# Optimization experiments

Hardware: AMD Instinct MI355X
Metric: run time of the kernel (lower is better)

## Reference

```python
import jax, jax.numpy as jnp
import numpy as np

BANDWIDTHS = (1e-2, 1e-1, 1e0, 1e1)  # params = [{'bandwidth': 10**i} for i in range(-2, 2)]


def setup_inputs() -> dict:
    key = jax.random.key(0)
    kx, ky = jax.random.split(key)
    n, d = 6144, 16
    X = jax.random.normal(kx, (n, d), dtype=jnp.float32)
    Y = jax.random.normal(ky, (n, d), dtype=jnp.float32)
    return {"X": X, "Y": Y}


def reference(X, Y):
    n_x, n_y = X.shape[0], Y.shape[0]
    M = jnp.concatenate([X, Y], axis=0)                     # [n_x+n_y, d]
    sq = jnp.sum(M * M, axis=1)                             # [N]
    D = sq[:, None] + sq[None, :] - 2.0 * (M @ M.T)         # squared pairwise dists [N,N]
    D = jnp.maximum(D, 0.0)
    # SumKernels over 4 RBF bandwidths: K = sum_b exp(-D / (2*bw^2))
    K = jnp.zeros_like(D)
    for bw in BANDWIDTHS:
        K = K + jnp.exp(-D / (2.0 * bw * bw))
    # cross_average biased mask S = outer(s, s) with s = [1/n_x,...,-1/n_y,...];
    # (S*K).sum() == s^T K s, computed without materializing S.
    s = jnp.concatenate([jnp.full((n_x,), 1.0 / n_x, dtype=M.dtype),
                         jnp.full((n_y,), -1.0 / n_y, dtype=M.dtype)])
    return jnp.einsum('i,ij,j->', s, K, s)
```

## Files before the change

### kernel.cpp

```cpp
#include <hip/hip_runtime.h>


using bf16x8 = __attribute__((ext_vector_type(8))) __bf16;
using f32x16 = __attribute__((ext_vector_type(16))) float;

constexpr int DIM   = 16;
constexpr int PTILE = 128;
constexpr int BLOCK = 256;
constexpr int CHUNK = 3;

constexpr float C1f = 0.72134752044448170f;
constexpr float C2f = 0.0072134752044448170f;

__device__ __forceinline__ float exp2_fast(float x) {
    float r; asm("v_exp_f32 %0, %1" : "=v"(r) : "v"(x)); return r;
}
__device__ __forceinline__ f32x16 zf() {
    f32x16 z;
#pragma unroll
    for (int i = 0; i < 16; ++i) z[i] = 0.f;
    return z;
}
__device__ __forceinline__ float sq4(float4 v) {
    return v.x*v.x + v.y*v.y + v.z*v.z + v.w*v.w;
}

__global__ __launch_bounds__(256) void mmd_prep(
    const float* __restrict__ X, const float* __restrict__ Y, int nx, int N,
    bf16x8* __restrict__ hi, bf16x8* __restrict__ lo, float* __restrict__ sq)
{
    int pt = blockIdx.x * blockDim.x + threadIdx.x;
    if (pt >= N) return;
    const float* row = (pt < nx) ? (X + (size_t)pt * DIM)
                                 : (Y + (size_t)(pt - nx) * DIM);
    const float4* r4 = reinterpret_cast<const float4*>(row);
    float4 u0 = r4[0], u1 = r4[1], u2 = r4[2], u3 = r4[3];
    float v[16] = {u0.x,u0.y,u0.z,u0.w, u1.x,u1.y,u1.z,u1.w,
                   u2.x,u2.y,u2.z,u2.w, u3.x,u3.y,u3.z,u3.w};
    float s = sq4(u0) + sq4(u1) + sq4(u2) + sq4(u3);

    bf16x8 H0, H1, L0, L1;
#pragma unroll
    for (int k = 0; k < 8; ++k) {
        __bf16 h0 = (__bf16)v[k];
        __bf16 h1 = (__bf16)v[k + 8];
        H0[k] = h0; H1[k] = h1;
        L0[k] = (__bf16)(v[k]     - (float)h0);
        L1[k] = (__bf16)(v[k + 8] - (float)h1);
    }
    int g = pt >> 5, p = pt & 31;
    hi[(g*2 + 0)*32 + p] = H0;
    hi[(g*2 + 1)*32 + p] = H1;
    lo[(g*2 + 0)*32 + p] = L0;
    lo[(g*2 + 1)*32 + p] = L1;
    sq[pt] = s;
}

struct Buf {
    bf16x8 aH0, aH1, aL0, aL1, bH0, bH1, bL0, bL1;
    float qa0[16], qa1[16];
    float qb0, qb1;
    float scale;
    int mode;
};

#define EPI_FULL(ACC, QA, QB) do { \
    _Pragma("unroll") \
    for (int q = 0; q < 16; ++q) { \
        float dd = fmaf(-2.f, ACC[q], QA[q] + QB); \
        accA += exp2_fast(-C1f * dd); \
        accB += exp2_fast(-C2f * dd); \
    } } while (0)

#define EPI_MASK(ACC, QA, QB) do { \
    _Pragma("unroll") \
    for (int q = 0; q < 16; ++q) { \
        float dd = fmaf(-2.f, ACC[q], QA[q] + QB); \
        float e1 = exp2_fast(-C1f * dd); \
        float e2 = exp2_fast(-C2f * dd); \
        bool m = l31 > (4*lh + (q & 3) + 8*(q >> 2)); \
        accA += m ? e1 : 0.f; \
        accB += m ? e2 : 0.f; \
    } } while (0)

__global__ __launch_bounds__(BLOCK, 2) void mmd_pairs3(
    const bf16x8* __restrict__ hi, const bf16x8* __restrict__ lo,
    const float*  __restrict__ sq, int nx, int T, int npairs,
    float wxf, float wynf, double* __restrict__ partials)
{
    __shared__ double wsums[BLOCK / 64];
    const int tid = threadIdx.x, w = tid >> 6, lane = tid & 63;
    const int wr = w >> 1, wc = w & 1, l31 = lane & 31, lh = lane >> 5;
    const int fo = lh * 32 + l31;

    float acc_run = 0.f;
    Buf B0, B1;

    auto issue = [&](int p, Buf& B) {
        if (p >= npairs) { B.mode = 3; return; }
        double A = (double)(2 * T + 1);
        int ti = (int)((A - sqrt(A * A - 8.0 * (double)p)) * 0.5);
        while ((ti + 1) * (2 * T + 1 - (ti + 1)) / 2 <= p) ++ti;
        while (ti * (2 * T + 1 - ti) / 2 > p) --ti;
        int tj = ti + (p - ti * (2 * T + 1 - ti) / 2);
        bool dg = (ti == tj);
        B.mode = dg ? ((wr > wc) ? 2 : ((wr == wc) ? 1 : 0)) : 0;
        int i0 = ti * PTILE, j0 = tj * PTILE;
        float wi = (i0 < nx) ? wxf : wynf;
        float wj = (j0 < nx) ? wxf : wynf;
        B.scale = wi * wj;
        if (B.mode == 2) return;
        int ga = ti * 4 + 2 * wr, gb = tj * 4 + 2 * wc;
        B.aH0 = hi[(ga + 0) * 64 + fo]; B.aH1 = hi[(ga + 1) * 64 + fo];
        B.aL0 = lo[(ga + 0) * 64 + fo]; B.aL1 = lo[(ga + 1) * 64 + fo];
        B.bH0 = hi[(gb + 0) * 64 + fo]; B.bH1 = hi[(gb + 1) * 64 + fo];
        B.bL0 = lo[(gb + 0) * 64 + fo]; B.bL1 = lo[(gb + 1) * 64 + fo];
        const float4* s4 = reinterpret_cast<const float4*>(sq);
        int rb0 = ((ga + 0) * 32 + 4 * lh) >> 2;
        int rb1 = ((ga + 1) * 32 + 4 * lh) >> 2;
        float4 t0 = s4[rb0 + 0], t1 = s4[rb0 + 2], t2 = s4[rb0 + 4], t3 = s4[rb0 + 6];
        float4 u0 = s4[rb1 + 0], u1 = s4[rb1 + 2], u2 = s4[rb1 + 4], u3 = s4[rb1 + 6];
        B.qa0[0]=t0.x;  B.qa0[1]=t0.y;  B.qa0[2]=t0.z;  B.qa0[3]=t0.w;
        B.qa0[4]=t1.x;  B.qa0[5]=t1.y;  B.qa0[6]=t1.z;  B.qa0[7]=t1.w;
        B.qa0[8]=t2.x;  B.qa0[9]=t2.y;  B.qa0[10]=t2.z; B.qa0[11]=t2.w;
        B.qa0[12]=t3.x; B.qa0[13]=t3.y; B.qa0[14]=t3.z; B.qa0[15]=t3.w;
        B.qa1[0]=u0.x;  B.qa1[1]=u0.y;  B.qa1[2]=u0.z;  B.qa1[3]=u0.w;
        B.qa1[4]=u1.x;  B.qa1[5]=u1.y;  B.qa1[6]=u1.z;  B.qa1[7]=u1.w;
        B.qa1[8]=u2.x;  B.qa1[9]=u2.y;  B.qa1[10]=u2.z; B.qa1[11]=u2.w;
        B.qa1[12]=u3.x; B.qa1[13]=u3.y; B.qa1[14]=u3.z; B.qa1[15]=u3.w;
        B.qb0 = sq[(gb + 0) * 32 + l31];
        B.qb1 = sq[(gb + 1) * 32 + l31];
    };

    auto compute = [&](Buf& B) {
        if (B.mode >= 2) return;
        f32x16 a00 = zf(), a01 = zf(), a10 = zf(), a11 = zf();
        a00 = __builtin_amdgcn_mfma_f32_32x32x16_bf16(B.aL0, B.bH0, a00, 0,0,0);
        a01 = __builtin_amdgcn_mfma_f32_32x32x16_bf16(B.aL0, B.bH1, a01, 0,0,0);
        a10 = __builtin_amdgcn_mfma_f32_32x32x16_bf16(B.aL1, B.bH0, a10, 0,0,0);
        a11 = __builtin_amdgcn_mfma_f32_32x32x16_bf16(B.aL1, B.bH1, a11, 0,0,0);
        a00 = __builtin_amdgcn_mfma_f32_32x32x16_bf16(B.aH0, B.bL0, a00, 0,0,0);
        a01 = __builtin_amdgcn_mfma_f32_32x32x16_bf16(B.aH0, B.bL1, a01, 0,0,0);
        a10 = __builtin_amdgcn_mfma_f32_32x32x16_bf16(B.aH1, B.bL0, a10, 0,0,0);
        a11 = __builtin_amdgcn_mfma_f32_32x32x16_bf16(B.aH1, B.bL1, a11, 0,0,0);
        a00 = __builtin_amdgcn_mfma_f32_32x32x16_bf16(B.aH0, B.bH0, a00, 0,0,0);
        a01 = __builtin_amdgcn_mfma_f32_32x32x16_bf16(B.aH0, B.bH1, a01, 0,0,0);
        a10 = __builtin_amdgcn_mfma_f32_32x32x16_bf16(B.aH1, B.bH0, a10, 0,0,0);
        a11 = __builtin_amdgcn_mfma_f32_32x32x16_bf16(B.aH1, B.bH1, a11, 0,0,0);

        float accA = 0.f, accB = 0.f;
        if (B.mode == 1) {
            EPI_MASK(a00, B.qa0, B.qb0);
            EPI_FULL(a01, B.qa0, B.qb1);
            EPI_MASK(a11, B.qa1, B.qb1);
        } else {
            EPI_FULL(a00, B.qa0, B.qb0);
            EPI_FULL(a01, B.qa0, B.qb1);
            EPI_FULL(a10, B.qa1, B.qb0);
            EPI_FULL(a11, B.qa1, B.qb1);
        }
        acc_run = fmaf(B.scale, accA + accB, acc_run);
    };

    const int base = blockIdx.x * CHUNK;
    issue(base + 0, B0);
    issue(base + 1, B1);
    compute(B0);
    issue(base + 2, B0);
    compute(B1);
    compute(B0);

    float tot = acc_run;
#pragma unroll
    for (int off = 32; off > 0; off >>= 1) tot += __shfl_down(tot, off);
    if (lane == 0) wsums[w] = (double)tot;
    __syncthreads();
    if (tid == 0)
        partials[blockIdx.x] = wsums[0] + wsums[1] + wsums[2] + wsums[3];
}

__global__ void mmd_reduce(const double* __restrict__ partials, int nb,
                           float* __restrict__ out, double diagv)
{
    __shared__ double sh[256];
    double s = 0.0;
    for (int i = threadIdx.x; i < nb; i += 256) s += partials[i];
    sh[threadIdx.x] = s;
    __syncthreads();
    for (int st = 128; st > 0; st >>= 1) {
        if (threadIdx.x < st) sh[threadIdx.x] += sh[threadIdx.x + st];
        __syncthreads();
    }
    if (threadIdx.x == 0) out[0] = (float)(2.0 * sh[0] + diagv);
}

__global__ void mmd_finalize(const double* __restrict__ acc,
                             float* __restrict__ out, double diag)
{
    out[0] = (float)(2.0 * acc[0] + diag);
}

constexpr int FTILE = 256;
constexpr int FBLOCK = 128;
__global__ __launch_bounds__(FBLOCK, 4) void mmd_pairs_fb(
    const float* __restrict__ Xp, const float* __restrict__ Yp,
    int nx, int T, double wx, double wyn, double* __restrict__ acc_out)
{
    __shared__ float  bs[FTILE][DIM];
    __shared__ float  bsq[FTILE];
    __shared__ double wsums[FBLOCK / 64];
    int ti = 0;
    int rem = blockIdx.x;
    while (rem >= T - ti) { rem -= (T - ti); ++ti; }
    int tj = ti + rem;
    const int i0 = ti * FTILE, j0 = tj * FTILE;
    const float* bbase = (j0 < nx) ? (Xp + (size_t)j0 * DIM) : (Yp + (size_t)(j0 - nx) * DIM);
    const float* abase = (i0 < nx) ? (Xp + (size_t)i0 * DIM) : (Yp + (size_t)(i0 - nx) * DIM);
    for (int r = threadIdx.x; r < FTILE; r += FBLOCK) {
        const float4* rp = reinterpret_cast<const float4*>(bbase + (size_t)r * DIM);
        float4 v0 = rp[0], v1 = rp[1], v2 = rp[2], v3 = rp[3];
        float4* sp = reinterpret_cast<float4*>(&bs[r][0]);
        sp[0]=v0; sp[1]=v1; sp[2]=v2; sp[3]=v3;
        bsq[r] = sq4(v0)+sq4(v1)+sq4(v2)+sq4(v3);
    }
    float a0[DIM], a1[DIM], sqa0, sqa1;
    {
        const float4* r0 = reinterpret_cast<const float4*>(abase + (size_t)threadIdx.x * DIM);
        const float4* r1 = reinterpret_cast<const float4*>(abase + (size_t)(threadIdx.x + FBLOCK) * DIM);
        float4 u0=r0[0],u1=r0[1],u2=r0[2],u3=r0[3];
        float4 v0=r1[0],v1=r1[1],v2=r1[2],v3=r1[3];
        float ta[16]={u0.x,u0.y,u0.z,u0.w,u1.x,u1.y,u1.z,u1.w,u2.x,u2.y,u2.z,u2.w,u3.x,u3.y,u3.z,u3.w};
        float tb[16]={v0.x,v0.y,v0.z,v0.w,v1.x,v1.y,v1.z,v1.w,v2.x,v2.y,v2.z,v2.w,v3.x,v3.y,v3.z,v3.w};
#pragma unroll
        for (int k=0;k<16;++k){a0[k]=ta[k];a1[k]=tb[k];}
        sqa0 = sq4(u0)+sq4(u1)+sq4(u2)+sq4(u3);
        sqa1 = sq4(v0)+sq4(v1)+sq4(v2)+sq4(v3);
    }
    __syncthreads();
    float acc0=0.f, acc1=0.f;
    const int ig0 = i0 + threadIdx.x, ig1 = ig0 + FBLOCK;
    for (int j = 0; j < FTILE; ++j) {
        float d0=0.f, d1=0.f;
#pragma unroll
        for (int k=0;k<DIM;++k){ float bk=bs[j][k]; d0=fmaf(a0[k],bk,d0); d1=fmaf(a1[k],bk,d1); }
        float sb=bsq[j];
        float dd0=fmaxf(fmaf(-2.f,d0,sqa0+sb),0.f);
        float dd1=fmaxf(fmaf(-2.f,d1,sqa1+sb),0.f);
        float e0=exp2_fast(-C1f*dd0)+exp2_fast(-C2f*dd0);
        float e1=exp2_fast(-C1f*dd1)+exp2_fast(-C2f*dd1);
        int jg=j0+j;
        bool full = (ti!=tj);
        acc0 += (full || jg>ig0)? e0:0.f;
        acc1 += (full || jg>ig1)? e1:0.f;
    }
    float tot=acc0+acc1;
#pragma unroll
    for (int off=32; off>0; off>>=1) tot += __shfl_down(tot,off);
    int wid=threadIdx.x>>6, lane=threadIdx.x&63;
    if (lane==0) wsums[wid]=(double)tot;
    __syncthreads();
    if (threadIdx.x==0){
        double s=0.0;
#pragma unroll
        for (int q=0;q<FBLOCK/64;++q) s+=wsums[q];
        double wi=(i0<nx)?wx:wyn, wj=(j0<nx)?wx:wyn;
        atomicAdd(acc_out, wi*wj*s);
    }
}

extern "C" void kernel_launch(void* const* d_in, const int* in_sizes, int n_in,
                              void* d_out, int out_size, void* d_ws, size_t ws_size,
                              hipStream_t stream)
{
    const float* X = (const float*)d_in[0];
    const float* Y = (const float*)d_in[1];
    int nx = in_sizes[0] / DIM;
    int ny = in_sizes[1] / DIM;
    int N  = nx + ny;
    double wx  = 1.0 / (double)nx;
    double wyn = -1.0 / (double)ny;
    double diagv = 4.0 * (1.0 / (double)nx + 1.0 / (double)ny);

    char* wsb = (char*)d_ws;

    int Tm = N / PTILE;
    int npairs = Tm * (Tm + 1) / 2;
    int NB = (npairs + CHUNK - 1) / CHUNK;

    size_t off_hi = 1024;
    size_t off_lo = off_hi + (size_t)N * DIM * 2;
    size_t off_sq = off_lo + (size_t)N * DIM * 2;
    size_t off_pt = off_sq + (size_t)N * 4;
    size_t need   = off_pt + (size_t)NB * 8;

    if (ws_size >= need && (N % PTILE) == 0 && (nx % PTILE) == 0) {
        bf16x8* hi  = (bf16x8*)(wsb + off_hi);
        bf16x8* lo  = (bf16x8*)(wsb + off_lo);
        float*  sqp = (float*) (wsb + off_sq);
        double* pts = (double*)(wsb + off_pt);
        mmd_prep<<<(N + 255) / 256, 256, 0, stream>>>(X, Y, nx, N, hi, lo, sqp);
        mmd_pairs3<<<NB, BLOCK, 0, stream>>>(hi, lo, sqp, nx, Tm, npairs,
                                             (float)wx, (float)wyn, pts);
        mmd_reduce<<<1, 256, 0, stream>>>(pts, NB, (float*)d_out, diagv);
    } else {
        double* acc = (double*)wsb;
        hipMemsetAsync(acc, 0, sizeof(double), stream);
        int T = N / FTILE;
        int nb = T * (T + 1) / 2;
        mmd_pairs_fb<<<nb, FBLOCK, 0, stream>>>(X, Y, nx, T, wx, wyn, acc);
        mmd_finalize<<<1, 1, 0, stream>>>(acc, (float*)d_out, diagv);
    }
}
```

Baseline: 43.84 us.

## Fold squared-norm terms into an extra MFMA and simplify epilogue

```diff
diff --git a/kernel.cpp b/kernel.cpp
--- a/kernel.cpp
+++ b/kernel.cpp
@@ -7,10 +7,10 @@
 constexpr int DIM   = 16;
 constexpr int PTILE = 128;
 constexpr int BLOCK = 256;
-constexpr int CHUNK = 3;
-
-constexpr float C1f = 0.72134752044448170f;
-constexpr float C2f = 0.0072134752044448170f;
+constexpr int CHUNK = 2;
+
+constexpr float K1f = 1.4426950408889634f;
+constexpr float K2f = 0.014426950408889634f;
 
 __device__ __forceinline__ float exp2_fast(float x) {
     float r; asm("v_exp_f32 %0, %1" : "=v"(r) : "v"(x)); return r;
@@ -26,8 +26,9 @@
 }
 
 __global__ __launch_bounds__(256) void mmd_prep(
-    const float* __restrict__ X, const float* __restrict__ Y, int nx, int N,
-    bf16x8* __restrict__ hi, bf16x8* __restrict__ lo, float* __restrict__ sq)
+    const float* __restrict__ X, const float* __restrict__ Y, int nx, int N, int G,
+    bf16x8* __restrict__ hi, bf16x8* __restrict__ lo,
+    bf16x8* __restrict__ sqA, bf16x8* __restrict__ sqB)
 {
     int pt = blockIdx.x * blockDim.x + threadIdx.x;
     if (pt >= N) return;
@@ -48,44 +49,52 @@
         L0[k] = (__bf16)(v[k]     - (float)h0);
         L1[k] = (__bf16)(v[k + 8] - (float)h1);
     }
+    float t  = -0.5f * s;
+    __bf16 p1 = (__bf16)t;  float r1 = t  - (float)p1;
+    __bf16 p2 = (__bf16)r1; float r2 = r1 - (float)p2;
+    __bf16 p3 = (__bf16)r2;
+    __bf16 one = (__bf16)1.0f, zb = (__bf16)0.0f;
+    bf16x8 SA = {p1, p2, p3, one, one, one, zb, zb};
+    bf16x8 SB = {one, one, one, p1, p2, p3, zb, zb};
+
     int g = pt >> 5, p = pt & 31;
     hi[(g*2 + 0)*32 + p] = H0;
     hi[(g*2 + 1)*32 + p] = H1;
     lo[(g*2 + 0)*32 + p] = L0;
     lo[(g*2 + 1)*32 + p] = L1;
-    sq[pt] = s;
-}
-
-struct Buf {
-    bf16x8 aH0, aH1, aL0, aL1, bH0, bH1, bL0, bL1;
-    float qa0[16], qa1[16];
-    float qb0, qb1;
-    float scale;
-    int mode;
-};
-
-#define EPI_FULL(ACC, QA, QB) do { \
-    _Pragma("unroll") \
+    sqA[g*32 + p] = SA;
+    sqB[g*32 + p] = SB;
+    if (pt < 32) {
+        bf16x8 Z = {zb,zb,zb,zb,zb,zb,zb,zb};
+        sqA[G*32 + pt] = Z;
+        sqB[G*32 + pt] = Z;
+    }
+}
+
+#define DOT4(C, AH, AL, SA_, BH, BL, SB_) \
+    C = __builtin_amdgcn_mfma_f32_32x32x16_bf16(AH,  BH,  C, 0,0,0); \
+    C = __builtin_amdgcn_mfma_f32_32x32x16_bf16(AL,  BH,  C, 0,0,0); \
+    C = __builtin_amdgcn_mfma_f32_32x32x16_bf16(AH,  BL,  C, 0,0,0); \
+    C = __builtin_amdgcn_mfma_f32_32x32x16_bf16(SA_, SB_, C, 0,0,0);
+
+#define EPI_FULL(C) do { _Pragma("unroll") \
     for (int q = 0; q < 16; ++q) { \
-        float dd = fmaf(-2.f, ACC[q], QA[q] + QB); \
-        accA += exp2_fast(-C1f * dd); \
-        accB += exp2_fast(-C2f * dd); \
+        float m = C[q]; \
+        accP += exp2_fast(K1f * m) + exp2_fast(K2f * m); \
     } } while (0)
 
-#define EPI_MASK(ACC, QA, QB) do { \
-    _Pragma("unroll") \
+#define EPI_MASK(C) do { _Pragma("unroll") \
     for (int q = 0; q < 16; ++q) { \
-        float dd = fmaf(-2.f, ACC[q], QA[q] + QB); \
-        float e1 = exp2_fast(-C1f * dd); \
-        float e2 = exp2_fast(-C2f * dd); \
-        bool m = l31 > (4*lh + (q & 3) + 8*(q >> 2)); \
-        accA += m ? e1 : 0.f; \
-        accB += m ? e2 : 0.f; \
+        float m = C[q]; \
+        float e = exp2_fast(K1f * m) + exp2_fast(K2f * m); \
+        bool msk = l31 > (4*lh + (q & 3) + 8*(q >> 2)); \
+        accP += msk ? e : 0.f; \
     } } while (0)
 
-__global__ __launch_bounds__(BLOCK, 2) void mmd_pairs3(
+__global__ __launch_bounds__(BLOCK, 4) void mmd_pairs4(
     const bf16x8* __restrict__ hi, const bf16x8* __restrict__ lo,
-    const float*  __restrict__ sq, int nx, int T, int npairs,
+    const bf16x8* __restrict__ sqA, const bf16x8* __restrict__ sqB,
+    int nx, int T, int G, int npairs,
     float wxf, float wynf, double* __restrict__ partials)
 {
     __shared__ double wsums[BLOCK / 64];
@@ -93,82 +102,58 @@
     const int wr = w >> 1, wc = w & 1, l31 = lane & 31, lh = lane >> 5;
     const int fo = lh * 32 + l31;
 
+    int p = blockIdx.x * CHUNK;
+    double Ad = (double)(2 * T + 1);
+    int ti = (int)((Ad - sqrt(Ad * Ad - 8.0 * (double)p)) * 0.5);
+    while ((ti + 1) * (2 * T + 1 - (ti + 1)) / 2 <= p) ++ti;
+    while (ti * (2 * T + 1 - ti) / 2 > p) --ti;
+    int tj = ti + (p - ti * (2 * T + 1 - ti) / 2);
+
     float acc_run = 0.f;
-    Buf B0, B1;
-
-    auto issue = [&](int p, Buf& B) {
-        if (p >= npairs) { B.mode = 3; return; }
-        double A = (double)(2 * T + 1);
-        int ti = (int)((A - sqrt(A * A - 8.0 * (double)p)) * 0.5);
-        while ((ti + 1) * (2 * T + 1 - (ti + 1)) / 2 <= p) ++ti;
-        while (ti * (2 * T + 1 - ti) / 2 > p) --ti;
-        int tj = ti + (p - ti * (2 * T + 1 - ti) / 2);
-        bool dg = (ti == tj);
-        B.mode = dg ? ((wr > wc) ? 2 : ((wr == wc) ? 1 : 0)) : 0;
-        int i0 = ti * PTILE, j0 = tj * PTILE;
-        float wi = (i0 < nx) ? wxf : wynf;
-        float wj = (j0 < nx) ? wxf : wynf;
-        B.scale = wi * wj;
-        if (B.mode == 2) return;
-        int ga = ti * 4 + 2 * wr, gb = tj * 4 + 2 * wc;
-        B.aH0 = hi[(ga + 0) * 64 + fo]; B.aH1 = hi[(ga + 1) * 64 + fo];
-        B.aL0 = lo[(ga + 0) * 64 + fo]; B.aL1 = lo[(ga + 1) * 64 + fo];
-        B.bH0 = hi[(gb + 0) * 64 + fo]; B.bH1 = hi[(gb + 1) * 64 + fo];
-        B.bL0 = lo[(gb + 0) * 64 + fo]; B.bL1 = lo[(gb + 1) * 64 + fo];
-        const float4* s4 = reinterpret_cast<const float4*>(sq);
-        int rb0 = ((ga + 0) * 32 + 4 * lh) >> 2;
-        int rb1 = ((ga + 1) * 32 + 4 * lh) >> 2;
-        float4 t0 = s4[rb0 + 0], t1 = s4[rb0 + 2], t2 = s4[rb0 + 4], t3 = s4[rb0 + 6];
-        float4 u0 = s4[rb1 + 0], u1 = s4[rb1 + 2], u2 = s4[rb1 + 4], u3 = s4[rb1 + 6];
-        B.qa0[0]=t0.x;  B.qa0[1]=t0.y;  B.qa0[2]=t0.z;  B.qa0[3]=t0.w;
-        B.qa0[4]=t1.x;  B.qa0[5]=t1.y;  B.qa0[6]=t1.z;  B.qa0[7]=t1.w;
-        B.qa0[8]=t2.x;  B.qa0[9]=t2.y;  B.qa0[10]=t2.z; B.qa0[11]=t2.w;
-        B.qa0[12]=t3.x; B.qa0[13]=t3.y; B.qa0[14]=t3.z; B.qa0[15]=t3.w;
-        B.qa1[0]=u0.x;  B.qa1[1]=u0.y;  B.qa1[2]=u0.z;  B.qa1[3]=u0.w;
-        B.qa1[4]=u1.x;  B.qa1[5]=u1.y;  B.qa1[6]=u1.z;  B.qa1[7]=u1.w;
-        B.qa1[8]=u2.x;  B.qa1[9]=u2.y;  B.qa1[10]=u2.z; B.qa1[11]=u2.w;
-        B.qa1[12]=u3.x; B.qa1[13]=u3.y; B.qa1[14]=u3.z; B.qa1[15]=u3.w;
-        B.qb0 = sq[(gb + 0) * 32 + l31];
-        B.qb1 = sq[(gb + 1) * 32 + l31];
-    };
-
-    auto compute = [&](Buf& B) {
-        if (B.mode >= 2) return;
-        f32x16 a00 = zf(), a01 = zf(), a10 = zf(), a11 = zf();
-        a00 = __builtin_amdgcn_mfma_f32_32x32x16_bf16(B.aL0, B.bH0, a00, 0,0,0);
-        a01 = __builtin_amdgcn_mfma_f32_32x32x16_bf16(B.aL0, B.bH1, a01, 0,0,0);
-        a10 = __builtin_amdgcn_mfma_f32_32x32x16_bf16(B.aL1, B.bH0, a10, 0,0,0);
-        a11 = __builtin_amdgcn_mfma_f32_32x32x16_bf16(B.aL1, B.bH1, a11, 0,0,0);
-        a00 = __builtin_amdgcn_mfma_f32_32x32x16_bf16(B.aH0, B.bL0, a00, 0,0,0);
-        a01 = __builtin_amdgcn_mfma_f32_32x32x16_bf16(B.aH0, B.bL1, a01, 0,0,0);
-        a10 = __builtin_amdgcn_mfma_f32_32x32x16_bf16(B.aH1, B.bL0, a10, 0,0,0);
-        a11 = __builtin_amdgcn_mfma_f32_32x32x16_bf16(B.aH1, B.bL1, a11, 0,0,0);
-        a00 = __builtin_amdgcn_mfma_f32_32x32x16_bf16(B.aH0, B.bH0, a00, 0,0,0);
-        a01 = __builtin_amdgcn_mfma_f32_32x32x16_bf16(B.aH0, B.bH1, a01, 0,0,0);
-        a10 = __builtin_amdgcn_mfma_f32_32x32x16_bf16(B.aH1, B.bH0, a10, 0,0,0);
-        a11 = __builtin_amdgcn_mfma_f32_32x32x16_bf16(B.aH1, B.bH1, a11, 0,0,0);
-
-        float accA = 0.f, accB = 0.f;
-        if (B.mode == 1) {
-            EPI_MASK(a00, B.qa0, B.qb0);
-            EPI_FULL(a01, B.qa0, B.qb1);
-            EPI_MASK(a11, B.qa1, B.qb1);
-        } else {
-            EPI_FULL(a00, B.qa0, B.qb0);
-            EPI_FULL(a01, B.qa0, B.qb1);
-            EPI_FULL(a10, B.qa1, B.qb0);
-            EPI_FULL(a11, B.qa1, B.qb1);
+
+    for (int c = 0; c < CHUNK; ++c) {
+        if (p + c < npairs) {
+            bool dg = (ti == tj);
+            int mode = dg ? ((wr > wc) ? 2 : ((wr == wc) ? 1 : 0)) : 0;
+            float wi = (ti * PTILE < nx) ? wxf : wynf;
+            float wj = (tj * PTILE < nx) ? wxf : wynf;
+            float scale = wi * wj;
+            if (mode != 2) {
+                int ga = ti * 4 + 2 * wr, gb = tj * 4 + 2 * wc;
+                bf16x8 aH0 = hi[(ga+0)*64 + fo], aH1 = hi[(ga+1)*64 + fo];
+                bf16x8 aL0 = lo[(ga+0)*64 + fo], aL1 = lo[(ga+1)*64 + fo];
+                bf16x8 bH0 = hi[(gb+0)*64 + fo], bH1 = hi[(gb+1)*64 + fo];
+                bf16x8 bL0 = lo[(gb+0)*64 + fo], bL1 = lo[(gb+1)*64 + fo];
+                bf16x8 sa0 = sqA[(lh ? G : ga+0)*32 + l31];
+                bf16x8 sa1 = sqA[(lh ? G : ga+1)*32 + l31];
+                bf16x8 sb0 = sqB[(lh ? G : gb+0)*32 + l31];
+                bf16x8 sb1 = sqB[(lh ? G : gb+1)*32 + l31];
+
+                float accP = 0.f;
+                if (mode == 0) {
+                    f32x16 c0 = zf(), c1 = zf(), c2 = zf(), c3 = zf();
+                    DOT4(c0, aH0, aL0, sa0, bH0, bL0, sb0);
+                    DOT4(c1, aH0, aL0, sa0, bH1, bL1, sb1);
+                    EPI_FULL(c0);
+                    DOT4(c2, aH1, aL1, sa1, bH0, bL0, sb0);
+                    EPI_FULL(c1);
+                    DOT4(c3, aH1, aL1, sa1, bH1, bL1, sb1);
+                    EPI_FULL(c2);
+                    EPI_FULL(c3);
+                } else {
+                    f32x16 c0 = zf(), c1 = zf(), c3 = zf();
+                    DOT4(c0, aH0, aL0, sa0, bH0, bL0, sb0);
+                    DOT4(c1, aH0, aL0, sa0, bH1, bL1, sb1);
+                    EPI_MASK(c0);
+                    DOT4(c3, aH1, aL1, sa1, bH1, bL1, sb1);
+                    EPI_FULL(c1);
+                    EPI_MASK(c3);
+                }
+                acc_run = fmaf(scale, accP, acc_run);
+            }
         }
-        acc_run = fmaf(B.scale, accA + accB, acc_run);
-    };
-
-    const int base = blockIdx.x * CHUNK;
-    issue(base + 0, B0);
-    issue(base + 1, B1);
-    compute(B0);
-    issue(base + 2, B0);
-    compute(B1);
-    compute(B0);
+        if (++tj == T) { ++ti; tj = ti; }
+    }
 
     float tot = acc_run;
 #pragma unroll
@@ -202,6 +187,8 @@
 
 constexpr int FTILE = 256;
 constexpr int FBLOCK = 128;
+constexpr float C1f = 0.72134752044448170f;
+constexpr float C2f = 0.0072134752044448170f;
 __global__ __launch_bounds__(FBLOCK, 4) void mmd_pairs_fb(
     const float* __restrict__ Xp, const float* __restrict__ Yp,
     int nx, int T, double wx, double wyn, double* __restrict__ acc_out)
@@ -283,23 +270,26 @@
 
     char* wsb = (char*)d_ws;
 
+    int G  = N / 32;
     int Tm = N / PTILE;
     int npairs = Tm * (Tm + 1) / 2;
     int NB = (npairs + CHUNK - 1) / CHUNK;
 
-    size_t off_hi = 1024;
-    size_t off_lo = off_hi + (size_t)N * DIM * 2;
-    size_t off_sq = off_lo + (size_t)N * DIM * 2;
-    size_t off_pt = off_sq + (size_t)N * 4;
-    size_t need   = off_pt + (size_t)NB * 8;
+    size_t off_hi  = 1024;
+    size_t off_lo  = off_hi  + (size_t)N * DIM * 2;
+    size_t off_sqA = off_lo  + (size_t)N * DIM * 2;
+    size_t off_sqB = off_sqA + (size_t)(G + 1) * 32 * 16;
+    size_t off_pt  = off_sqB + (size_t)(G + 1) * 32 * 16;
+    size_t need    = off_pt  + (size_t)NB * 8;
 
     if (ws_size >= need && (N % PTILE) == 0 && (nx % PTILE) == 0) {
         bf16x8* hi  = (bf16x8*)(wsb + off_hi);
         bf16x8* lo  = (bf16x8*)(wsb + off_lo);
-        float*  sqp = (float*) (wsb + off_sq);
+        bf16x8* sqA = (bf16x8*)(wsb + off_sqA);
+        bf16x8* sqB = (bf16x8*)(wsb + off_sqB);
         double* pts = (double*)(wsb + off_pt);
-        mmd_prep<<<(N + 255) / 256, 256, 0, stream>>>(X, Y, nx, N, hi, lo, sqp);
-        mmd_pairs3<<<NB, BLOCK, 0, stream>>>(hi, lo, sqp, nx, Tm, npairs,
+        mmd_prep<<<(N + 255) / 256, 256, 0, stream>>>(X, Y, nx, N, G, hi, lo, sqA, sqB);
+        mmd_pairs4<<<NB, BLOCK, 0, stream>>>(hi, lo, sqA, sqB, nx, Tm, G, npairs,
                                              (float)wx, (float)wyn, pts);
         mmd_reduce<<<1, 256, 0, stream>>>(pts, NB, (float*)d_out, diagv);
     } else {
```

Result: faster. 38.64 us (-11.9%).
